# Optimization experiments

Measured on AMD Instinct MI355X. Metric: run time of the kernel, lower is better.

Reference implementation:

```python
import jax, jax.numpy as jnp
import numpy as np
import math

D_EMBED = 128   # per-head dim (config.d_embed)
N_HEADS = 12
ROPE_BASE = 10000.0


def rope(x):
    # x: [B, H, S, D]; interleaved-pair rotary embedding on last dim
    B, H, S, D = x.shape
    half = D // 2
    inv_freq = 1.0 / (ROPE_BASE ** (jnp.arange(0, half, dtype=jnp.float32) * 2.0 / D))
    ang = jnp.arange(S, dtype=jnp.float32)[:, None] * inv_freq[None, :]  # [S, D/2]
    cos, sin = jnp.cos(ang), jnp.sin(ang)
    xp = x.reshape(B, H, S, half, 2)
    x1, x2 = xp[..., 0], xp[..., 1]
    o1 = x1 * cos - x2 * sin
    o2 = x1 * sin + x2 * cos
    return jnp.stack([o1, o2], axis=-1).reshape(B, H, S, D)


def setup_inputs() -> dict:
    key = jax.random.key(0)
    ks = jax.random.split(key, 5)
    B, S, E = 2, 2048, D_EMBED // 2
    inner = N_HEADS * D_EMBED
    sc = 0.02
    return {
        "q": jax.random.normal(ks[0], (B, S, E), dtype=jnp.float32),
        "Wq": jax.random.normal(ks[1], (inner, E), dtype=jnp.float32) * sc,
        "Wk": jax.random.normal(ks[2], (inner, E), dtype=jnp.float32) * sc,
        "Wv": jax.random.normal(ks[3], (inner, E), dtype=jnp.float32) * sc,
        "Wo": jax.random.normal(ks[4], (E, inner), dtype=jnp.float32) * sc,
    }


def reference(q, Wq, Wk, Wv, Wo):
    B, S, E = q.shape
    H, D = N_HEADS, D_EMBED
    scale = 1.0 / math.sqrt(D)

    def proj(x, W):
        return (x @ W.T).reshape(B, S, H, D).transpose(0, 2, 1, 3)  # [B,H,S,D]

    qh = rope(proj(q, Wq))
    kh = rope(proj(q, Wk))
    vh = proj(q, Wv)

    scores = jnp.einsum("bhsd,bhtd->bhst", qh, kh) * scale  # [B,H,S,S]
    causal = jnp.tril(jnp.ones((S, S), dtype=bool))
    scores = jnp.where(causal, scores, -jnp.inf)
    probs = jax.nn.softmax(scores, axis=-1)  # dropout omitted (eval mode)
    out = jnp.einsum("bhst,bhtd->bhsd", probs, vh)
    out = out.transpose(0, 2, 1, 3).reshape(B, S, H * D)
    return out @ Wo.T  # [B,S,E]
```

## Files before the change

### kernel.cpp

```cpp
#include <hip/hip_runtime.h>
#include <stdint.h>


typedef short v8s __attribute__((ext_vector_type(8)));
typedef unsigned int v4u __attribute__((ext_vector_type(4)));
typedef float v4f __attribute__((ext_vector_type(4)));
typedef float v16f __attribute__((ext_vector_type(16)));

#define MFMA16(a, b, c) __builtin_amdgcn_mfma_f32_16x16x32_bf16(a, b, c, 0, 0, 0)
#define MFMA32(a, b, c) __builtin_amdgcn_mfma_f32_32x32x16_bf16(a, b, c, 0, 0, 0)

#if __has_builtin(__builtin_amdgcn_exp2f)
#define EXP2(x) __builtin_amdgcn_exp2f(x)
#else
#define EXP2(x) exp2f(x)
#endif

#define SCALE2 (0.08838834764831845f * 1.4426950408889634f)

__device__ __forceinline__ unsigned short f2bf(float f) {
  uint32_t u = __builtin_bit_cast(uint32_t, f);
  u += 0x7FFFu + ((u >> 16) & 1u);
  return (unsigned short)(u >> 16);
}

__device__ __forceinline__ uint32_t packbf(float lo, float hi) {
  return __builtin_amdgcn_perm(__builtin_bit_cast(uint32_t, hi) + 0x8000u,
                               __builtin_bit_cast(uint32_t, lo) + 0x8000u,
                               0x07060302u);
}

__device__ __forceinline__ v16f zero16() {
  v16f z;
#pragma unroll
  for (int i = 0; i < 16; ++i) z[i] = 0.f;
  return z;
}

__device__ __forceinline__ void gl_lds16(const unsigned short* g, unsigned short* l) {
  __builtin_amdgcn_global_load_lds(
      (const __attribute__((address_space(1))) uint32_t*)g,
      (__attribute__((address_space(3))) uint32_t*)l, 16, 0, 0);
}

__global__ __launch_bounds__(256) void rope_table(float* __restrict__ cos_t,
                                                  float* __restrict__ sin_t) {
  int idx = blockIdx.x * 256 + threadIdx.x;
  if (idx >= 2048 * 64) return;
  int s = idx >> 6, f = idx & 63;
  float inv = exp2f((float)f * -0.20762050593046014f);
  float ang = (float)s * inv;
  float si, co;
  sincosf(ang, &si, &co);
  cos_t[idx] = co;
  sin_t[idx] = si;
}

__global__ __launch_bounds__(256) void proj_rope(
    const float* __restrict__ x, const float* __restrict__ Wq,
    const float* __restrict__ Wk, const float* __restrict__ Wv,
    const float* __restrict__ cos_t, const float* __restrict__ sin_t,
    unsigned short* __restrict__ qh, unsigned short* __restrict__ kh,
    unsigned short* __restrict__ vt) {
  const int wave = threadIdx.x >> 6, lane = threadIdx.x & 63;
  const int l16 = lane & 15, quad = lane >> 4;
  const int by = blockIdx.y;
  const int o_base = by * 64 + wave * 16;
  const int mat = o_base / 1536;
  const int inner0 = o_base % 1536;
  const int d0w = inner0 & 127;
  const float* Wsrc = (mat == 0) ? Wq : ((mat == 1) ? Wk : Wv);
  const float qscale = (mat == 0) ? SCALE2 : 1.0f;

  __shared__ __align__(16) unsigned short Lt[64][72];

  v8s wb[2];
  {
    const float* wr = Wsrc + (size_t)(inner0 + l16) * 64 + quad * 8;
#pragma unroll
    for (int s = 0; s < 2; ++s) {
      float4 a = *(const float4*)(wr + s * 32);
      float4 b = *(const float4*)(wr + s * 32 + 4);
      v8s t;
      t[0] = (short)f2bf(a.x); t[1] = (short)f2bf(a.y);
      t[2] = (short)f2bf(a.z); t[3] = (short)f2bf(a.w);
      t[4] = (short)f2bf(b.x); t[5] = (short)f2bf(b.y);
      t[6] = (short)f2bf(b.z); t[7] = (short)f2bf(b.w);
      wb[s] = t;
    }
  }

  const int d = d0w + l16;
  const int half = d >> 1;

#pragma unroll
  for (int i = 0; i < 4; ++i) {
    const int tok0 = blockIdx.x * 64 + i * 16;
    const float* xr = x + (size_t)(tok0 + l16) * 64 + quad * 8;
    v8s xa[2];
#pragma unroll
    for (int s = 0; s < 2; ++s) {
      float4 a = *(const float4*)(xr + s * 32);
      float4 b = *(const float4*)(xr + s * 32 + 4);
      v8s t;
      t[0] = (short)f2bf(a.x); t[1] = (short)f2bf(a.y);
      t[2] = (short)f2bf(a.z); t[3] = (short)f2bf(a.w);
      t[4] = (short)f2bf(b.x); t[5] = (short)f2bf(b.y);
      t[6] = (short)f2bf(b.z); t[7] = (short)f2bf(b.w);
      xa[s] = t;
    }
    v4f acc = {0.f, 0.f, 0.f, 0.f};
    acc = MFMA16(xa[0], wb[0], acc);
    acc = MFMA16(xa[1], wb[1], acc);

    if (mat < 2) {
#pragma unroll
      for (int r = 0; r < 4; ++r) {
        int sidx = (tok0 + quad * 4 + r) & 2047;
        float val = acc[r];
        float prt = __shfl_xor(val, 1);
        float co = cos_t[sidx * 64 + half];
        float si = sin_t[sidx * 64 + half];
        float rot = ((d & 1) == 0) ? (val * co - prt * si)
                                   : (prt * si + val * co);
        Lt[i * 16 + quad * 4 + r][wave * 16 + l16] = f2bf(rot * qscale);
      }
    } else {
#pragma unroll
      for (int r = 0; r < 4; ++r)
        Lt[wave * 16 + l16][i * 16 + quad * 4 + r] = f2bf(acc[r]);
    }
  }
  __syncthreads();

  const int matb = (by * 64) / 1536;
  const int innerb = (by * 64) % 1536;
  const int hb = innerb >> 7;
  const int d0b = innerb & 127;
  const int b = (blockIdx.x * 64) >> 11;
  const int tokbase = (blockIdx.x * 64) & 2047;
#pragma unroll
  for (int jj = 0; jj < 2; ++jj) {
    int cid = jj * 256 + threadIdx.x;
    int outer = cid >> 3, ic = cid & 7;
    v8s val = *(const v8s*)&Lt[outer][ic * 8];
    if (matb < 2) {
      unsigned short* dst = (matb == 0 ? qh : kh) +
          (((size_t)(b * 12 + hb)) * 2048 + tokbase + outer) * 128 + d0b + ic * 8;
      *(v8s*)dst = val;
    } else {
      unsigned short* dst = vt +
          (((size_t)(b * 12 + hb)) * 128 + d0b + outer) * 2048 + tokbase + ic * 8;
      *(v8s*)dst = val;
    }
  }
}

__global__ __launch_bounds__(256, 2) void attn(
    const unsigned short* __restrict__ qh, const unsigned short* __restrict__ kh,
    const unsigned short* __restrict__ vt, unsigned short* __restrict__ att,
    const float* __restrict__ Wo, unsigned short* __restrict__ wob) {
  const int bh = blockIdx.x;
  const int qb = 15 - (int)blockIdx.y;
  const int t = threadIdx.x;
  const int lane = t & 63;
  const int l31 = lane & 31, hh = lane >> 5;
  const int w = t >> 6;
  const int r0w = qb * 128 + w * 32;
  const int qrow = r0w + l31;
  const int rowmax = r0w + 31;

  const unsigned short* Qb = qh + (size_t)bh * 2048 * 128;
  const unsigned short* Kb = kh + (size_t)bh * 2048 * 128;
  const unsigned short* Vb = vt + (size_t)bh * 128 * 2048;

  __shared__ __align__(16) unsigned short Ktile[2][64 * 128];
  __shared__ __align__(16) unsigned short Vtile[2][128 * 64];

  v8s qa[8];
  {
    const unsigned short* qr = Qb + (size_t)(r0w + l31) * 128 + hh * 8;
#pragma unroll
    for (int ks = 0; ks < 8; ++ks) qa[ks] = *(const v8s*)(qr + ks * 16);
  }

  int offK[4], offV[4], ldsO[4];
#pragma unroll
  for (int j = 0; j < 4; ++j) {
    int flat = j * 256 + t;
    int kr = flat >> 4, kc = flat & 15;
    offK[j] = kr * 128 + ((kc ^ (kr & 15)) << 3);
    int vd = flat >> 3, vc = flat & 7;
    offV[j] = vd * 2048 + ((vc ^ (vd & 7)) << 3);
    ldsO[j] = flat << 3;
  }
  auto stage = [&](int kt, int buf) {
    const int key0 = kt << 6;
    const unsigned short* kg = Kb + (size_t)key0 * 128;
    const unsigned short* vg = Vb + key0;
#pragma unroll
    for (int j = 0; j < 4; ++j) {
      gl_lds16(kg + offK[j], &Ktile[buf][ldsO[j]]);
      gl_lds16(vg + offV[j], &Vtile[buf][ldsO[j]]);
    }
  };

  v16f O[4];
#pragma unroll
  for (int i = 0; i < 4; ++i) O[i] = zero16();
  float lsum = 0.f;

  const int nkt = 2 * qb + 2;
  stage(0, 0);

  for (int kt = 0; kt < nkt; ++kt) {
    __syncthreads();
    if (kt + 1 < nkt) stage(kt + 1, (kt + 1) & 1);
    const int key0 = kt << 6;
    if (key0 > rowmax) continue;
    const unsigned short* Kl = Ktile[kt & 1];
    const unsigned short* Vl = Vtile[kt & 1];
    const bool hi = (key0 + 32) <= rowmax;
    const bool mask0 = (key0 + 31) > r0w;
    const bool mask1 = (key0 + 63) > r0w;

    auto softpack = [&](const v16f& S, int kh2, bool needmask, uint32_t* W) {
#pragma unroll
      for (int m = 0; m < 8; ++m) {
        float pa = EXP2(S[2 * m]);
        float pb = EXP2(S[2 * m + 1]);
        if (needmask) {
          int keyb = key0 + kh2 * 32 + 2 * (m & 1) + 8 * (m >> 1) + 4 * hh;
          pa = (keyb <= qrow) ? pa : 0.f;
          pb = (keyb + 1 <= qrow) ? pb : 0.f;
        }
        lsum += pa + pb;
        W[m] = packbf(pa, pb);
      }
    };
    auto pv = [&](const uint32_t* W, int kh2) {
      uint32_t r0 = __shfl_xor(hh ? W[0] : W[2], 32);
      uint32_t r1 = __shfl_xor(hh ? W[1] : W[3], 32);
      uint32_t r2 = __shfl_xor(hh ? W[4] : W[6], 32);
      uint32_t r3 = __shfl_xor(hh ? W[5] : W[7], 32);
#pragma unroll
      for (int gl = 0; gl < 2; ++gl) {
        const int g = kh2 * 2 + gl;
        if (key0 + g * 16 > rowmax) continue;
        uint32_t rA = gl ? r2 : r0, rB = gl ? r3 : r1;
        v4u fw;
        fw.x = hh ? rA : W[4 * gl];
        fw.y = hh ? rB : W[4 * gl + 1];
        fw.z = hh ? W[4 * gl + 2] : rA;
        fw.w = hh ? W[4 * gl + 3] : rB;
        v8s pb = __builtin_bit_cast(v8s, fw);
#pragma unroll
        for (int dt = 0; dt < 4; ++dt) {
          v8s va = *(const v8s*)(
              Vl + (((dt * 32 + l31) * 8 + ((2 * g + hh) ^ (l31 & 7))) << 3));
          O[dt] = MFMA32(va, pb, O[dt]);
        }
      }
    };

    v16f S0 = zero16();
#pragma unroll
    for (int ks = 0; ks < 8; ++ks) {
      v8s ka = *(const v8s*)(
          Kl + ((l31 * 16 + ((2 * ks + hh) ^ (l31 & 15))) << 3));
      S0 = MFMA32(ka, qa[ks], S0);
    }
    uint32_t W0[8];
    softpack(S0, 0, mask0, W0);
    pv(W0, 0);
    if (hi) {
      v16f S1 = zero16();
#pragma unroll
      for (int ks = 0; ks < 8; ++ks) {
        v8s ka = *(const v8s*)(
            Kl + (((32 + l31) * 16 + ((2 * ks + hh) ^ (l31 & 15))) << 3));
        S1 = MFMA32(ka, qa[ks], S1);
      }
      uint32_t W1[8];
      softpack(S1, 1, mask1, W1);
      pv(W1, 1);
    }
  }

  float tot = lsum + __shfl_xor(lsum, 32);
  float inv = 1.0f / tot;
  const int b = bh / 12, hq = bh % 12;
  unsigned short* arow = att + ((size_t)b * 2048 + qrow) * 1536 + hq * 128;
#pragma unroll
  for (int dt = 0; dt < 4; ++dt) {
#pragma unroll
    for (int pr = 0; pr < 4; ++pr) {
      float a0 = O[dt][4 * pr + 0] * inv, a1 = O[dt][4 * pr + 1] * inv;
      float a2 = O[dt][4 * pr + 2] * inv, a3 = O[dt][4 * pr + 3] * inv;
      uint2 uu;
      uu.x = packbf(a0, a1);
      uu.y = packbf(a2, a3);
      *(uint2*)(arow + dt * 32 + 8 * pr + 4 * hh) = uu;
    }
  }

  if (qb == 0) {
    const int base = bh * 4096;
#pragma unroll
    for (int i = 0; i < 16; ++i) wob[base + i * 256 + t] = f2bf(Wo[base + i * 256 + t]);
  }
}

__global__ __launch_bounds__(256) void outproj(
    const unsigned short* __restrict__ att, const unsigned short* __restrict__ wob,
    float* __restrict__ out) {
  const int wave = threadIdx.x >> 6, lane = threadIdx.x & 63;
  const int l16 = lane & 15, quad = lane >> 4;
  const int tok0 = blockIdx.x * 16;
  const int e0 = wave * 16;

  v4f acc0 = {0.f, 0.f, 0.f, 0.f}, acc1 = {0.f, 0.f, 0.f, 0.f};
  const unsigned short* ar = att + (size_t)(tok0 + l16) * 1536 + quad * 8;
  const unsigned short* wr = wob + (size_t)(e0 + l16) * 1536 + quad * 8;
#pragma unroll 4
  for (int s = 0; s < 24; ++s) {
    v8s a0 = *(const v8s*)(ar + (2 * s) * 32);
    v8s b0 = *(const v8s*)(wr + (2 * s) * 32);
    v8s a1 = *(const v8s*)(ar + (2 * s + 1) * 32);
    v8s b1 = *(const v8s*)(wr + (2 * s + 1) * 32);
    acc0 = MFMA16(a0, b0, acc0);
    acc1 = MFMA16(a1, b1, acc1);
  }
#pragma unroll
  for (int r = 0; r < 4; ++r)
    out[(size_t)(tok0 + quad * 4 + r) * 64 + e0 + l16] = acc0[r] + acc1[r];
}

extern "C" void kernel_launch(void* const* d_in, const int* in_sizes, int n_in,
                              void* d_out, int out_size, void* d_ws,
                              size_t ws_size, hipStream_t stream) {
  const float* q  = (const float*)d_in[0];
  const float* Wq = (const float*)d_in[1];
  const float* Wk = (const float*)d_in[2];
  const float* Wv = (const float*)d_in[3];
  const float* Wo = (const float*)d_in[4];
  float* out = (float*)d_out;

  unsigned short* ws = (unsigned short*)d_ws;
  unsigned short* qh  = ws;
  unsigned short* kh  = ws + 6291456;
  unsigned short* vt  = ws + 12582912;
  unsigned short* att = ws + 18874368;
  float* cos_t = (float*)((char*)d_ws + 50331648);
  float* sin_t = cos_t + 131072;
  unsigned short* wob = (unsigned short*)cos_t;

  rope_table<<<512, 256, 0, stream>>>(cos_t, sin_t);
  proj_rope<<<dim3(64, 72), 256, 0, stream>>>(q, Wq, Wk, Wv, cos_t, sin_t,
                                              qh, kh, vt);
  attn<<<dim3(24, 16), 256, 0, stream>>>(qh, kh, vt, att, Wo, wob);
  outproj<<<256, 256, 0, stream>>>(att, wob, out);
}
```

Measured before the change: 191.9 us.

## Halve attention KV tile for higher occupancy, split-K out-projection with atomics

The attention kernel moves from 64-key to 32-key tiles, halving LDS use and raising launch bounds to 4 blocks per SM so more waves can be resident, at the cost of twice as many loop iterations and barriers. The output projection is split across two K halves, with each half accumulated into a zeroed output by atomicAdd, doubling the block count; this adds a memset and atomic traffic. The projection kernel's float-to-bf16 conversion now uses the packed perm helper, which rounds slightly differently.

```diff
diff --git a/kernel.cpp b/kernel.cpp
--- a/kernel.cpp
+++ b/kernel.cpp
@@ -28,6 +28,15 @@
   return __builtin_amdgcn_perm(__builtin_bit_cast(uint32_t, hi) + 0x8000u,
                                __builtin_bit_cast(uint32_t, lo) + 0x8000u,
                                0x07060302u);
+}
+
+__device__ __forceinline__ v8s cvt8(const float4& a, const float4& b) {
+  v4u u;
+  u.x = packbf(a.x, a.y);
+  u.y = packbf(a.z, a.w);
+  u.z = packbf(b.x, b.y);
+  u.w = packbf(b.z, b.w);
+  return __builtin_bit_cast(v8s, u);
 }
 
 __device__ __forceinline__ v16f zero16() {
@@ -78,16 +87,8 @@
   {
     const float* wr = Wsrc + (size_t)(inner0 + l16) * 64 + quad * 8;
 #pragma unroll
-    for (int s = 0; s < 2; ++s) {
-      float4 a = *(const float4*)(wr + s * 32);
-      float4 b = *(const float4*)(wr + s * 32 + 4);
-      v8s t;
-      t[0] = (short)f2bf(a.x); t[1] = (short)f2bf(a.y);
-      t[2] = (short)f2bf(a.z); t[3] = (short)f2bf(a.w);
-      t[4] = (short)f2bf(b.x); t[5] = (short)f2bf(b.y);
-      t[6] = (short)f2bf(b.z); t[7] = (short)f2bf(b.w);
-      wb[s] = t;
-    }
+    for (int s = 0; s < 2; ++s)
+      wb[s] = cvt8(*(const float4*)(wr + s * 32), *(const float4*)(wr + s * 32 + 4));
   }
 
   const int d = d0w + l16;
@@ -99,16 +100,8 @@
     const float* xr = x + (size_t)(tok0 + l16) * 64 + quad * 8;
     v8s xa[2];
 #pragma unroll
-    for (int s = 0; s < 2; ++s) {
-      float4 a = *(const float4*)(xr + s * 32);
-      float4 b = *(const float4*)(xr + s * 32 + 4);
-      v8s t;
-      t[0] = (short)f2bf(a.x); t[1] = (short)f2bf(a.y);
-      t[2] = (short)f2bf(a.z); t[3] = (short)f2bf(a.w);
-      t[4] = (short)f2bf(b.x); t[5] = (short)f2bf(b.y);
-      t[6] = (short)f2bf(b.z); t[7] = (short)f2bf(b.w);
-      xa[s] = t;
-    }
+    for (int s = 0; s < 2; ++s)
+      xa[s] = cvt8(*(const float4*)(xr + s * 32), *(const float4*)(xr + s * 32 + 4));
     v4f acc = {0.f, 0.f, 0.f, 0.f};
     acc = MFMA16(xa[0], wb[0], acc);
     acc = MFMA16(xa[1], wb[1], acc);
@@ -156,7 +149,7 @@
   }
 }
 
-__global__ __launch_bounds__(256, 2) void attn(
+__global__ __launch_bounds__(256, 4) void attn(
     const unsigned short* __restrict__ qh, const unsigned short* __restrict__ kh,
     const unsigned short* __restrict__ vt, unsigned short* __restrict__ att,
     const float* __restrict__ Wo, unsigned short* __restrict__ wob) {
@@ -174,8 +167,8 @@
   const unsigned short* Kb = kh + (size_t)bh * 2048 * 128;
   const unsigned short* Vb = vt + (size_t)bh * 128 * 2048;
 
-  __shared__ __align__(16) unsigned short Ktile[2][64 * 128];
-  __shared__ __align__(16) unsigned short Vtile[2][128 * 64];
+  __shared__ __align__(16) unsigned short Ktile[2][32 * 128];
+  __shared__ __align__(16) unsigned short Vtile[2][128 * 32];
 
   v8s qa[8];
   {
@@ -184,22 +177,22 @@
     for (int ks = 0; ks < 8; ++ks) qa[ks] = *(const v8s*)(qr + ks * 16);
   }
 
-  int offK[4], offV[4], ldsO[4];
-#pragma unroll
-  for (int j = 0; j < 4; ++j) {
+  int offK[2], offV[2], ldsO[2];
+#pragma unroll
+  for (int j = 0; j < 2; ++j) {
     int flat = j * 256 + t;
     int kr = flat >> 4, kc = flat & 15;
     offK[j] = kr * 128 + ((kc ^ (kr & 15)) << 3);
-    int vd = flat >> 3, vc = flat & 7;
-    offV[j] = vd * 2048 + ((vc ^ (vd & 7)) << 3);
+    int vd = flat >> 2, vc = flat & 3;
+    offV[j] = vd * 2048 + ((vc ^ (vd & 3)) << 3);
     ldsO[j] = flat << 3;
   }
   auto stage = [&](int kt, int buf) {
-    const int key0 = kt << 6;
+    const int key0 = kt << 5;
     const unsigned short* kg = Kb + (size_t)key0 * 128;
     const unsigned short* vg = Vb + key0;
 #pragma unroll
-    for (int j = 0; j < 4; ++j) {
+    for (int j = 0; j < 2; ++j) {
       gl_lds16(kg + offK[j], &Ktile[buf][ldsO[j]]);
       gl_lds16(vg + offV[j], &Vtile[buf][ldsO[j]]);
     }
@@ -210,58 +203,17 @@
   for (int i = 0; i < 4; ++i) O[i] = zero16();
   float lsum = 0.f;
 
-  const int nkt = 2 * qb + 2;
+  const int nkt = 4 * qb + 4;
   stage(0, 0);
 
   for (int kt = 0; kt < nkt; ++kt) {
     __syncthreads();
     if (kt + 1 < nkt) stage(kt + 1, (kt + 1) & 1);
-    const int key0 = kt << 6;
+    const int key0 = kt << 5;
     if (key0 > rowmax) continue;
     const unsigned short* Kl = Ktile[kt & 1];
     const unsigned short* Vl = Vtile[kt & 1];
-    const bool hi = (key0 + 32) <= rowmax;
-    const bool mask0 = (key0 + 31) > r0w;
-    const bool mask1 = (key0 + 63) > r0w;
-
-    auto softpack = [&](const v16f& S, int kh2, bool needmask, uint32_t* W) {
-#pragma unroll
-      for (int m = 0; m < 8; ++m) {
-        float pa = EXP2(S[2 * m]);
-        float pb = EXP2(S[2 * m + 1]);
-        if (needmask) {
-          int keyb = key0 + kh2 * 32 + 2 * (m & 1) + 8 * (m >> 1) + 4 * hh;
-          pa = (keyb <= qrow) ? pa : 0.f;
-          pb = (keyb + 1 <= qrow) ? pb : 0.f;
-        }
-        lsum += pa + pb;
-        W[m] = packbf(pa, pb);
-      }
-    };
-    auto pv = [&](const uint32_t* W, int kh2) {
-      uint32_t r0 = __shfl_xor(hh ? W[0] : W[2], 32);
-      uint32_t r1 = __shfl_xor(hh ? W[1] : W[3], 32);
-      uint32_t r2 = __shfl_xor(hh ? W[4] : W[6], 32);
-      uint32_t r3 = __shfl_xor(hh ? W[5] : W[7], 32);
-#pragma unroll
-      for (int gl = 0; gl < 2; ++gl) {
-        const int g = kh2 * 2 + gl;
-        if (key0 + g * 16 > rowmax) continue;
-        uint32_t rA = gl ? r2 : r0, rB = gl ? r3 : r1;
-        v4u fw;
-        fw.x = hh ? rA : W[4 * gl];
-        fw.y = hh ? rB : W[4 * gl + 1];
-        fw.z = hh ? W[4 * gl + 2] : rA;
-        fw.w = hh ? W[4 * gl + 3] : rB;
-        v8s pb = __builtin_bit_cast(v8s, fw);
-#pragma unroll
-        for (int dt = 0; dt < 4; ++dt) {
-          v8s va = *(const v8s*)(
-              Vl + (((dt * 32 + l31) * 8 + ((2 * g + hh) ^ (l31 & 7))) << 3));
-          O[dt] = MFMA32(va, pb, O[dt]);
-        }
-      }
-    };
+    const bool needmask = (key0 + 31) > r0w;
 
     v16f S0 = zero16();
 #pragma unroll
@@ -270,20 +222,41 @@
           Kl + ((l31 * 16 + ((2 * ks + hh) ^ (l31 & 15))) << 3));
       S0 = MFMA32(ka, qa[ks], S0);
     }
+
     uint32_t W0[8];
-    softpack(S0, 0, mask0, W0);
-    pv(W0, 0);
-    if (hi) {
-      v16f S1 = zero16();
-#pragma unroll
-      for (int ks = 0; ks < 8; ++ks) {
-        v8s ka = *(const v8s*)(
-            Kl + (((32 + l31) * 16 + ((2 * ks + hh) ^ (l31 & 15))) << 3));
-        S1 = MFMA32(ka, qa[ks], S1);
+#pragma unroll
+    for (int m = 0; m < 8; ++m) {
+      float pa = EXP2(S0[2 * m]);
+      float pb = EXP2(S0[2 * m + 1]);
+      if (needmask) {
+        int keyb = key0 + 2 * (m & 1) + 8 * (m >> 1) + 4 * hh;
+        pa = (keyb <= qrow) ? pa : 0.f;
+        pb = (keyb + 1 <= qrow) ? pb : 0.f;
       }
-      uint32_t W1[8];
-      softpack(S1, 1, mask1, W1);
-      pv(W1, 1);
+      lsum += pa + pb;
+      W0[m] = packbf(pa, pb);
+    }
+
+    uint32_t r0 = __shfl_xor(hh ? W0[0] : W0[2], 32);
+    uint32_t r1 = __shfl_xor(hh ? W0[1] : W0[3], 32);
+    uint32_t r2 = __shfl_xor(hh ? W0[4] : W0[6], 32);
+    uint32_t r3 = __shfl_xor(hh ? W0[5] : W0[7], 32);
+#pragma unroll
+    for (int gl = 0; gl < 2; ++gl) {
+      if (key0 + gl * 16 > rowmax) continue;
+      uint32_t rA = gl ? r2 : r0, rB = gl ? r3 : r1;
+      v4u fw;
+      fw.x = hh ? rA : W0[4 * gl];
+      fw.y = hh ? rB : W0[4 * gl + 1];
+      fw.z = hh ? W0[4 * gl + 2] : rA;
+      fw.w = hh ? W0[4 * gl + 3] : rB;
+      v8s pb = __builtin_bit_cast(v8s, fw);
+#pragma unroll
+      for (int dt = 0; dt < 4; ++dt) {
+        int kd = dt * 32 + l31;
+        v8s va = *(const v8s*)(Vl + ((kd * 4 + ((2 * gl + hh) ^ (kd & 3))) << 3));
+        O[dt] = MFMA32(va, pb, O[dt]);
+      }
     }
   }
 
@@ -318,22 +291,32 @@
   const int l16 = lane & 15, quad = lane >> 4;
   const int tok0 = blockIdx.x * 16;
   const int e0 = wave * 16;
+  const int koff = blockIdx.y * 768;
 
   v4f acc0 = {0.f, 0.f, 0.f, 0.f}, acc1 = {0.f, 0.f, 0.f, 0.f};
-  const unsigned short* ar = att + (size_t)(tok0 + l16) * 1536 + quad * 8;
-  const unsigned short* wr = wob + (size_t)(e0 + l16) * 1536 + quad * 8;
-#pragma unroll 4
-  for (int s = 0; s < 24; ++s) {
-    v8s a0 = *(const v8s*)(ar + (2 * s) * 32);
-    v8s b0 = *(const v8s*)(wr + (2 * s) * 32);
-    v8s a1 = *(const v8s*)(ar + (2 * s + 1) * 32);
-    v8s b1 = *(const v8s*)(wr + (2 * s + 1) * 32);
+  v4f acc2 = {0.f, 0.f, 0.f, 0.f}, acc3 = {0.f, 0.f, 0.f, 0.f};
+  const unsigned short* ar = att + (size_t)(tok0 + l16) * 1536 + koff + quad * 8;
+  const unsigned short* wr = wob + (size_t)(e0 + l16) * 1536 + koff + quad * 8;
+#pragma unroll 2
+  for (int s = 0; s < 6; ++s) {
+    v8s a0 = *(const v8s*)(ar + (4 * s) * 32);
+    v8s b0 = *(const v8s*)(wr + (4 * s) * 32);
+    v8s a1 = *(const v8s*)(ar + (4 * s + 1) * 32);
+    v8s b1 = *(const v8s*)(wr + (4 * s + 1) * 32);
+    v8s a2 = *(const v8s*)(ar + (4 * s + 2) * 32);
+    v8s b2 = *(const v8s*)(wr + (4 * s + 2) * 32);
+    v8s a3 = *(const v8s*)(ar + (4 * s + 3) * 32);
+    v8s b3 = *(const v8s*)(wr + (4 * s + 3) * 32);
     acc0 = MFMA16(a0, b0, acc0);
     acc1 = MFMA16(a1, b1, acc1);
-  }
-#pragma unroll
-  for (int r = 0; r < 4; ++r)
-    out[(size_t)(tok0 + quad * 4 + r) * 64 + e0 + l16] = acc0[r] + acc1[r];
+    acc2 = MFMA16(a2, b2, acc2);
+    acc3 = MFMA16(a3, b3, acc3);
+  }
+#pragma unroll
+  for (int r = 0; r < 4; ++r) {
+    float v = (acc0[r] + acc1[r]) + (acc2[r] + acc3[r]);
+    atomicAdd(&out[(size_t)(tok0 + quad * 4 + r) * 64 + e0 + l16], v);
+  }
 }
 
 extern "C" void kernel_launch(void* const* d_in, const int* in_sizes, int n_in,
@@ -359,5 +342,6 @@
   proj_rope<<<dim3(64, 72), 256, 0, stream>>>(q, Wq, Wk, Wv, cos_t, sin_t,
                                               qh, kh, vt);
   attn<<<dim3(24, 16), 256, 0, stream>>>(qh, kh, vt, att, Wo, wob);
-  outproj<<<256, 256, 0, stream>>>(att, wob, out);
-}
+  hipMemsetAsync(out, 0, (size_t)out_size * sizeof(float), stream);
+  outproj<<<dim3(256, 2), 256, 0, stream>>>(att, wob, out);
+}
```

After: 266.2 us. 1.39x slower.
